# Optimization experiments

Measured on AMD Instinct MI355X. Metric: run time of the kernel, lower is better.

## Reference

```python
import jax, jax.numpy as jnp
import numpy as np

B, N, K = 2, 16384, 8
NH, HD, CH, KV_IN = 4, 32, 128, 128
EPS = 1e-5

def layer_norm(x, g, b):
    mu = x.mean(-1, keepdims=True)
    var = ((x - mu) ** 2).mean(-1, keepdims=True)
    return (x - mu) / jnp.sqrt(var + EPS) * g + b

def setup_inputs() -> dict:
    key = jax.random.key(0)
    ks = jax.random.split(key, 8)
    s = 0.02
    return {
        "query_in": jax.random.normal(ks[0], (B, N, CH), jnp.float32),
        "kv_in": jax.random.normal(ks[1], (B, N, K, KV_IN), jnp.float32),
        "w_kv": jax.random.normal(ks[2], (KV_IN, 2 * NH * HD), jnp.float32) * s,
        "w_q": jax.random.normal(ks[3], (CH, NH * HD), jnp.float32) * s,
        "w_mh": jax.random.normal(ks[4], (NH * HD, CH), jnp.float32) * s,
        "b_mh": jnp.zeros((CH,), jnp.float32),
        "w1": jax.random.normal(ks[5], (CH, CH), jnp.float32) * s,
        "b1": jnp.zeros((CH,), jnp.float32),
        "w2": jax.random.normal(ks[6], (CH, CH), jnp.float32) * s,
        "b2": jnp.zeros((CH,), jnp.float32),
        "ln1_g": jnp.ones((CH,), jnp.float32),
        "ln1_b": jnp.zeros((CH,), jnp.float32),
        "ln2_g": jnp.ones((CH,), jnp.float32),
        "ln2_b": jnp.zeros((CH,), jnp.float32),
    }

def reference(query_in, kv_in, w_kv, w_q, w_mh, b_mh, w1, b1, w2, b2,
              ln1_g, ln1_b, ln2_g, ln2_b):
    # q projection: [B,N,CH] -> [B,N,NH,HD]
    q = (query_in @ w_q).reshape(B, N, NH, HD)
    # kv projection: [B,N,K,KV_IN] -> [B,N,K,2,NH,HD]; chunk(2) on last dim
    kv = (kv_in @ w_kv).reshape(B, N, K, 2, NH, HD)
    k, v = kv[..., 0, :, :], kv[..., 1, :, :]  # each [B,N,K,NH,HD]
    # per-token local attention over its own K keys
    sim = jnp.einsum('bnhd,bnkhd->bnhk', q, k) / np.sqrt(HD).astype(np.float32)
    attn = jax.nn.softmax(sim, axis=-1)
    out = jnp.einsum('bnhk,bnkhd->bnhd', attn, v).reshape(B, N, NH * HD)
    out = out @ w_mh + b_mh
    res = layer_norm(out, ln1_g, ln1_b) + query_in
    # GELU MLP (torch nn.GELU default = exact erf form)
    mlp = jax.nn.gelu(res @ w1 + b1, approximate=False) @ w2 + b2
    return layer_norm(mlp + res, ln2_g, ln2_b)
```

## Files before the change

kernel.cpp:

```cpp
#include <hip/hip_runtime.h>
#include <hip/hip_fp16.h>

typedef _Float16 f16x8 __attribute__((ext_vector_type(8)));
typedef float f32x4 __attribute__((ext_vector_type(4)));
typedef unsigned int uint32;

#define LDW 136
#define TB  32

#define WAITLGKM() do { __builtin_amdgcn_s_waitcnt(0xC07F); __builtin_amdgcn_sched_barrier(0); } while(0)

#define BAR() do {                                          \
  asm volatile("s_waitcnt lgkmcnt(0)" ::: "memory");        \
  __builtin_amdgcn_sched_barrier(0);                        \
  __builtin_amdgcn_s_barrier();                             \
  __builtin_amdgcn_sched_barrier(0);                        \
} while (0)

union F16x8U { f16x8 v; __half2 h2[4]; uint2 u2[2]; uint4 u4; };

__device__ __forceinline__ uint32 pk2f(float a, float b) {
  __half2 h = __floats2half2_rn(a, b);
  return *reinterpret_cast<uint32*>(&h);
}
__device__ __forceinline__ float bcast(float v, int sl) {
  return __int_as_float(__builtin_amdgcn_readlane(__float_as_int(v), sl));
}
template <int CTRL, int RMASK = 0xF, int BMASK = 0xF>
__device__ __forceinline__ float dppmov(float v) {
  return __int_as_float(__builtin_amdgcn_update_dpp(
      0, __float_as_int(v), CTRL, RMASK, BMASK, true));
}
template <int PAT>
__device__ __forceinline__ float swzf(float v) {
  return __int_as_float(__builtin_amdgcn_ds_swizzle(__float_as_int(v), PAT));
}
__device__ __forceinline__ float wred_sum(float v) {
  v += dppmov<0x111>(v);
  v += dppmov<0x112>(v);
  v += dppmov<0x114>(v);
  v += dppmov<0x118>(v);
  v += dppmov<0x142, 0xA>(v);
  v += dppmov<0x143, 0xC>(v);
  return __int_as_float(__builtin_amdgcn_readlane(__float_as_int(v), 63));
}
__device__ __forceinline__ f16x8 ldsv8(const __half* p) {
  return *reinterpret_cast<const f16x8*>(p);
}
__device__ __forceinline__ f32x4 mfma16(f16x8 a, f16x8 b, f32x4 c) {
  return __builtin_amdgcn_mfma_f32_16x16x32_f16(a, b, c, 0, 0, 0);
}
__device__ __forceinline__ void stp(__half* base, int fr, int fq, int nt, f32x4 a) {
  uint2 u; u.x = pk2f(a[0], a[1]); u.y = pk2f(a[2], a[3]);
  *reinterpret_cast<uint2*>(&base[fr * LDW + nt * 16 + fq * 4]) = u;
}

#define OFF_WQ   0
#define OFF_WK2  16384
#define OFF_WV   36864
#define OFF_WMH  53248
#define OFF_W1   69632
#define OFF_W2   86016
#define WS_HALVES 102400

__global__ void prep_weights(const float* __restrict__ wq, const float* __restrict__ wkv,
                             const float* __restrict__ wmh, const float* __restrict__ w1,
                             const float* __restrict__ w2, __half* __restrict__ ws) {
  int idx = blockIdx.x * 256 + threadIdx.x;
  if (idx >= WS_HALVES) return;
  float v;
  if (idx < OFF_WK2) {
    int t = idx, c = t >> 7, k = t & 127;
    v = wq[k * 128 + c];
  } else if (idx < OFF_WV) {
    int t = idx - OFF_WK2;
    int d = t % 40, row = t / 40;
    int h = row >> 7, i = row & 127;
    v = (d < 32) ? wkv[i * 256 + h * 32 + d] : 0.f;
  } else if (idx < OFF_WMH) {
    int t = idx - OFF_WV, c = t >> 7, k = t & 127;
    v = wkv[k * 256 + 128 + c];
  } else if (idx < OFF_W1) {
    int t = idx - OFF_WMH, c = t >> 7, k = t & 127;
    v = wmh[k * 128 + c];
  } else if (idx < OFF_W2) {
    int t = idx - OFF_W1, c = t >> 7, k = t & 127;
    v = w1[k * 128 + c];
  } else {
    int t = idx - OFF_W2, c = t >> 7, k = t & 127;
    v = w2[k * 128 + c];
  }
  ws[idx] = __float2half_rn(v);
}

#define LOADB2(GOFF, NT0, NT1, BF) do {                                          \
  _Pragma("unroll")                                                              \
  for (int t_ = 0; t_ < 2; ++t_) {                                               \
    int nt_ = t_ ? (NT1) : (NT0);                                                \
    _Pragma("unroll")                                                            \
    for (int ks_ = 0; ks_ < 4; ++ks_)                                            \
      BF[t_][ks_] = *reinterpret_cast<const f16x8*>(                             \
          wsv + (GOFF) + (nt_*16 + fr)*128 + ks_*32 + fq*8);                     \
  } } while (0)

#define GEMM2(AT, BF, ACC0, ACC1) do {                                           \
  _Pragma("unroll")                                                              \
  for (int ks_ = 0; ks_ < 4; ++ks_) {                                            \
    f16x8 b_ = ldsv8(&(AT)[fr * LDW + ks_ * 32 + fq * 8]);                       \
    ACC0 = mfma16(BF[0][ks_], b_, ACC0);                                         \
    ACC1 = mfma16(BF[1][ks_], b_, ACC1);                                         \
  } } while (0)

__global__ void __launch_bounds__(256, 3) ca_mfma(
    const float* __restrict__ xq, const float* __restrict__ kvin,
    const __half* __restrict__ wsv,
    const float* __restrict__ bmh, const float* __restrict__ b1,
    const float* __restrict__ b2,
    const float* __restrict__ g1, const float* __restrict__ bb1,
    const float* __restrict__ g2, const float* __restrict__ bb2,
    float* __restrict__ outp)
{
  __shared__ __half QWC[2 * 64 * LDW];
  __shared__ __half UBUF[2 * 32 * LDW];

  const int tid = threadIdx.x;
  const int wv = tid >> 6, lane = tid & 63;
  const int fr = lane & 15, fq = lane >> 4;
  const int tb = blockIdx.x * TB;
  const int ltb = wv * 4;

  __half* const QWs[2] = {QWC, QWC + 64 * LDW};
  __half* const Us[2]  = {UBUF, UBUF + 32 * LDW};

  const f32x4 ZZ = {0.f, 0.f, 0.f, 0.f};

  float4 pre[2][4];
#pragma unroll
  for (int st = 0; st < 2; ++st) {
    const float4* kv4 = reinterpret_cast<const float4*>(
        kvin + (size_t)(tb + st * 16 + ltb) * 1024);
    pre[st][0] = kv4[2 * lane];       pre[st][1] = kv4[2 * lane + 1];
    pre[st][2] = kv4[2 * lane + 128]; pre[st][3] = kv4[2 * lane + 129];
  }
  f16x8 bf[2][4];
  LOADB2(OFF_WQ, wv, 4 + wv, bf);

  {
    int tok = tid >> 4, ko = (tid & 15) * 8;
#pragma unroll
    for (int st = 0; st < 2; ++st) {
      const float4* s0 = reinterpret_cast<const float4*>(
          xq + (size_t)(tb + st * 16 + tok) * 128 + ko);
      float4 a = s0[0], b = s0[1];
      uint4 u; u.x = pk2f(a.x, a.y); u.y = pk2f(a.z, a.w);
      u.z = pk2f(b.x, b.y); u.w = pk2f(b.z, b.w);
      *reinterpret_cast<uint4*>(&Us[st][tok * LDW + ko]) = u;
    }
  }
  BAR();

#pragma unroll
  for (int st = 0; st < 2; ++st) {
    f32x4 aA = ZZ, aB = ZZ;
    GEMM2(Us[st], bf, aA, aB);
    stp(Us[st] + 16 * LDW, fr, fq, wv, aA);
    stp(Us[st] + 16 * LDW, fr, fq, 4 + wv, aB);
  }
  f16x8 bq[8];
#pragma unroll
  for (int nt = 0; nt < 8; ++nt)
    bq[nt] = *reinterpret_cast<const f16x8*>(
        wsv + OFF_WK2 + (wv * 128 + nt * 16 + fr) * 40 + fq * 8);
  BAR();

#pragma unroll
  for (int st = 0; st < 2; ++st) {
    f16x8 aq = ldsv8(&Us[st][16 * LDW + fr * LDW + wv * 32 + fq * 8]);
#pragma unroll
    for (int nt = 0; nt < 8; ++nt) {
      f32x4 acc = mfma16(bq[nt], aq, ZZ);
      uint2 u; u.x = pk2f(acc[0], acc[1]); u.y = pk2f(acc[2], acc[3]);
      *reinterpret_cast<uint2*>(&QWs[st][(wv * 16 + fr) * LDW + nt * 16 + fq * 4]) = u;
    }
  }
  BAR();

  {
    const int kr = lane >> 4, i8 = (lane & 15) * 8;
    const int l2 = 2 * lane;
    const float SCALE = 0.17677669529663687f;
#pragma unroll 1
    for (int lt = 0; lt < 4; ++lt) {
      const int ltok = ltb + lt;
      WAITLGKM();
#pragma unroll
      for (int st = 0; st < 2; ++st) {
        __half* kvw = Us[st] + wv * 1088;
        uint4 u0, u1;
        u0.x = pk2f(pre[st][0].x, pre[st][0].y); u0.y = pk2f(pre[st][0].z, pre[st][0].w);
        u0.z = pk2f(pre[st][1].x, pre[st][1].y); u0.w = pk2f(pre[st][1].z, pre[st][1].w);
        u1.x = pk2f(pre[st][2].x, pre[st][2].y); u1.y = pk2f(pre[st][2].z, pre[st][2].w);
        u1.z = pk2f(pre[st][3].x, pre[st][3].y); u1.w = pk2f(pre[st][3].z, pre[st][3].w);
        *reinterpret_cast<uint4*>(&kvw[kr * LDW + i8]) = u0;
        *reinterpret_cast<uint4*>(&kvw[(4 + kr) * LDW + i8]) = u1;
      }
      if (lt < 3) {
#pragma unroll
        for (int st = 0; st < 2; ++st) {
          const float4* kv4 = reinterpret_cast<const float4*>(
              kvin + (size_t)(tb + st * 16 + ltok + 1) * 1024);
          pre[st][0] = kv4[2 * lane];       pre[st][1] = kv4[2 * lane + 1];
          pre[st][2] = kv4[2 * lane + 128]; pre[st][3] = kv4[2 * lane + 129];
        }
      }
      WAITLGKM();
      f32x4 acc[2];
#pragma unroll
      for (int st = 0; st < 2; ++st) {
        __half* kvw = Us[st] + wv * 1088;
        f32x4 a = ZZ;
#pragma unroll
        for (int ks = 0; ks < 4; ++ks) {
          f16x8 a_ = ldsv8(&QWs[st][((fr & 3) * 16 + ltok) * LDW + ks * 32 + fq * 8]);
          f16x8 b_ = ldsv8(&kvw[(fr & 7) * LDW + ks * 32 + fq * 8]);
          a = mfma16(a_, b_, a);
        }
        acc[st] = a;
      }
      float at_[2][4];
#pragma unroll
      for (int st = 0; st < 2; ++st) {
#pragma unroll
        for (int r = 0; r < 4; ++r) {
          float s = acc[st][r] * SCALE;
          float mx = fmaxf(s, dppmov<0xB1>(s));
          mx = fmaxf(mx, dppmov<0x4E>(mx));
          mx = fmaxf(mx, swzf<0x101F>(mx));
          float e = __expf(s - mx);
          float dn = e + dppmov<0xB1>(e);
          dn += dppmov<0x4E>(dn);
          dn += swzf<0x101F>(dn);
          at_[st][r] = __fdividef(e, dn);
        }
      }
#pragma unroll
      for (int st = 0; st < 2; ++st) {
        __half* kvw = Us[st] + wv * 1088;
        __half2 kvc[8];
#pragma unroll
        for (int k = 0; k < 8; ++k)
          kvc[k] = *reinterpret_cast<const __half2*>(&kvw[k * LDW + l2]);
#pragma unroll
        for (int h = 0; h < 4; ++h) {
          float c0 = 0.f, c1 = 0.f;
#pragma unroll
          for (int k = 0; k < 8; ++k) {
            float a = bcast(at_[st][h], k);
            float2 kf = __half22float2(kvc[k]);
            c0 = fmaf(a, kf.x, c0);
            c1 = fmaf(a, kf.y, c1);
          }
          *reinterpret_cast<__half2*>(&QWs[st][(h * 16 + ltok) * LDW + l2]) =
              __floats2half2_rn(c0, c1);
        }
      }
    }
  }
  LOADB2(OFF_WV, wv, 4 + wv, bf);
  BAR();

  float2 xr[2][4];
#pragma unroll
  for (int st = 0; st < 2; ++st)
#pragma unroll
    for (int lt = 0; lt < 4; ++lt) {
      int tok = tb + st * 16 + ltb + lt;
      xr[st][lt] = *reinterpret_cast<const float2*>(&xq[(size_t)tok * 128 + 2 * lane]);
    }
  {
    const int h1 = wv >> 1, h2 = 2 + (wv >> 1);
#pragma unroll
    for (int st = 0; st < 2; ++st) {
      f32x4 a1c = ZZ, a2c = ZZ;
#pragma unroll
      for (int ks = 0; ks < 4; ++ks) {
        f16x8 b1f = ldsv8(&QWs[st][(h1 * 16 + fr) * LDW + ks * 32 + fq * 8]);
        a1c = mfma16(bf[0][ks], b1f, a1c);
        f16x8 b2f = ldsv8(&QWs[st][(h2 * 16 + fr) * LDW + ks * 32 + fq * 8]);
        a2c = mfma16(bf[1][ks], b2f, a2c);
      }
      stp(Us[st], fr, fq, wv, a1c);
      stp(Us[st], fr, fq, 4 + wv, a2c);
    }
  }
  LOADB2(OFF_WMH, wv, 4 + wv, bf);
  BAR();

#pragma unroll
  for (int st = 0; st < 2; ++st) {
    f32x4 aA = ZZ, aB = ZZ;
    GEMM2(Us[st], bf, aA, aB);
    stp(QWs[st], fr, fq, wv, aA);
    stp(QWs[st], fr, fq, 4 + wv, aB);
  }
  LOADB2(OFF_W1, wv, 4 + wv, bf);
  BAR();

  {
    const int l2 = 2 * lane;
    float2 bm = *reinterpret_cast<const float2*>(&bmh[l2]);
    float2 gg = *reinterpret_cast<const float2*>(&g1[l2]);
    float2 cc = *reinterpret_cast<const float2*>(&bb1[l2]);
#pragma unroll
    for (int st = 0; st < 2; ++st)
#pragma unroll
      for (int lt = 0; lt < 4; ++lt) {
        int row = ltb + lt;
        float2 y = __half22float2(
            *reinterpret_cast<const __half2*>(&QWs[st][row * LDW + l2]));
        float v0 = y.x + bm.x, v1 = y.y + bm.y;
        float s = wred_sum(v0 + v1);
        float sq = wred_sum(v0 * v0 + v1 * v1);
        float mu = s * 0.0078125f;
        float var = sq * 0.0078125f - mu * mu;
        float rstd = rsqrtf(var + 1e-5f);
        float r0 = (v0 - mu) * rstd * gg.x + cc.x + xr[st][lt].x;
        float r1 = (v1 - mu) * rstd * gg.y + cc.y + xr[st][lt].y;
        *reinterpret_cast<__half2*>(&QWs[st][(16 + row) * LDW + l2]) =
            __floats2half2_rn(r0, r1);
      }
  }
  BAR();

  {
    int c0 = wv * 16 + fq * 4, c1 = 64 + wv * 16 + fq * 4;
    float4 b1a = *reinterpret_cast<const float4*>(&b1[c0]);
    float4 b1b = *reinterpret_cast<const float4*>(&b1[c1]);
#pragma unroll
    for (int st = 0; st < 2; ++st) {
      f32x4 aA = ZZ, aB = ZZ;
      GEMM2(QWs[st] + 16 * LDW, bf, aA, aB);
      uint2 ua, ub;
      float t0, t1;
      t0 = aA[0] + b1a.x; t0 = 0.5f * t0 * (1.f + erff(t0 * 0.70710678118654752f));
      t1 = aA[1] + b1a.y; t1 = 0.5f * t1 * (1.f + erff(t1 * 0.70710678118654752f));
      ua.x = pk2f(t0, t1);
      t0 = aA[2] + b1a.z; t0 = 0.5f * t0 * (1.f + erff(t0 * 0.70710678118654752f));
      t1 = aA[3] + b1a.w; t1 = 0.5f * t1 * (1.f + erff(t1 * 0.70710678118654752f));
      ua.y = pk2f(t0, t1);
      t0 = aB[0] + b1b.x; t0 = 0.5f * t0 * (1.f + erff(t0 * 0.70710678118654752f));
      t1 = aB[1] + b1b.y; t1 = 0.5f * t1 * (1.f + erff(t1 * 0.70710678118654752f));
      ub.x = pk2f(t0, t1);
      t0 = aB[2] + b1b.z; t0 = 0.5f * t0 * (1.f + erff(t0 * 0.70710678118654752f));
      t1 = aB[3] + b1b.w; t1 = 0.5f * t1 * (1.f + erff(t1 * 0.70710678118654752f));
      ub.y = pk2f(t0, t1);
      *reinterpret_cast<uint2*>(&QWs[st][(32 + fr) * LDW + c0]) = ua;
      *reinterpret_cast<uint2*>(&QWs[st][(32 + fr) * LDW + c1]) = ub;
    }
  }
  LOADB2(OFF_W2, wv, 4 + wv, bf);
  BAR();

  {
    int c0 = wv * 16 + fq * 4, c1 = 64 + wv * 16 + fq * 4;
    float4 b2a = *reinterpret_cast<const float4*>(&b2[c0]);
    float4 b2b = *reinterpret_cast<const float4*>(&b2[c1]);
#pragma unroll
    for (int st = 0; st < 2; ++st) {
      f32x4 aA = ZZ, aB = ZZ;
      GEMM2(QWs[st] + 32 * LDW, bf, aA, aB);
      F16x8U ra, rb;
      ra.u2[0] = *reinterpret_cast<const uint2*>(&QWs[st][(16 + fr) * LDW + c0]);
      rb.u2[0] = *reinterpret_cast<const uint2*>(&QWs[st][(16 + fr) * LDW + c1]);
      uint2 ua, ub;
      float2 p0 = __half22float2(ra.h2[0]), p1 = __half22float2(ra.h2[1]);
      ua.x = pk2f(aA[0] + b2a.x + p0.x, aA[1] + b2a.y + p0.y);
      ua.y = pk2f(aA[2] + b2a.z + p1.x, aA[3] + b2a.w + p1.y);
      float2 p2 = __half22float2(rb.h2[0]), p3 = __half22float2(rb.h2[1]);
      ub.x = pk2f(aB[0] + b2b.x + p2.x, aB[1] + b2b.y + p2.y);
      ub.y = pk2f(aB[2] + b2b.z + p3.x, aB[3] + b2b.w + p3.y);
      *reinterpret_cast<uint2*>(&QWs[st][(48 + fr) * LDW + c0]) = ua;
      *reinterpret_cast<uint2*>(&QWs[st][(48 + fr) * LDW + c1]) = ub;
    }
  }
  BAR();

  {
    const int l2 = 2 * lane;
    float2 gg = *reinterpret_cast<const float2*>(&g2[l2]);
    float2 cc = *reinterpret_cast<const float2*>(&bb2[l2]);
#pragma unroll
    for (int st = 0; st < 2; ++st)
#pragma unroll
      for (int lt = 0; lt < 4; ++lt) {
        int row = ltb + lt, tok = tb + st * 16 + row;
        float2 v = __half22float2(
            *reinterpret_cast<const __half2*>(&QWs[st][(48 + row) * LDW + l2]));
        float s = wred_sum(v.x + v.y);
        float sq = wred_sum(v.x * v.x + v.y * v.y);
        float mu = s * 0.0078125f;
        float var = sq * 0.0078125f - mu * mu;
        float rstd = rsqrtf(var + 1e-5f);
        float2 o;
        o.x = (v.x - mu) * rstd * gg.x + cc.x;
        o.y = (v.y - mu) * rstd * gg.y + cc.y;
        *reinterpret_cast<float2*>(&outp[(size_t)tok * 128 + l2]) = o;
      }
  }
}

extern "C" void kernel_launch(void* const* d_in, const int* in_sizes, int n_in,
                              void* d_out, int out_size, void* d_ws, size_t ws_size,
                              hipStream_t stream) {
  const float* xq = (const float*)d_in[0];
  const float* kv = (const float*)d_in[1];
  const float* wkv = (const float*)d_in[2];
  const float* wq = (const float*)d_in[3];
  const float* wmh = (const float*)d_in[4];
  const float* bmh = (const float*)d_in[5];
  const float* w1 = (const float*)d_in[6];
  const float* b1 = (const float*)d_in[7];
  const float* w2 = (const float*)d_in[8];
  const float* b2 = (const float*)d_in[9];
  const float* g1 = (const float*)d_in[10];
  const float* bb1 = (const float*)d_in[11];
  const float* g2 = (const float*)d_in[12];
  const float* bb2 = (const float*)d_in[13];
  __half* ws = (__half*)d_ws;

  prep_weights<<<(WS_HALVES + 255) / 256, 256, 0, stream>>>(wq, wkv, wmh, w1, w2, ws);

  const int tokens = 32768;
  ca_mfma<<<tokens / TB, 256, 0, stream>>>(xq, kv, ws, bmh, b1, b2,
                                           g1, bb1, g2, bb2, (float*)d_out);
}
```

Measured before the change: 54.43 us.

## Fuse LayerNorms into MFMA epilogues with cross-wave partial sums in LDS

Both LayerNorms are now computed directly from the MFMA accumulator registers. Each wave reduces its column slice with a swizzle and a shuffle, writes per-row partial sums to a small LDS array, and finalizes after a barrier. This removes the fp16 round-trip through LDS, the separate per-token full-wave DPP reductions and one barrier per LayerNorm. The Q-projection column assignment is changed so each wave produces the columns it consumes next, which lets one block barrier become a local lgkm wait. It also relies on the column mapping being exactly right and adds a small LDS buffer.

```diff
diff --git a/kernel.cpp b/kernel.cpp
--- a/kernel.cpp
+++ b/kernel.cpp
@@ -34,15 +34,6 @@
 template <int PAT>
 __device__ __forceinline__ float swzf(float v) {
   return __int_as_float(__builtin_amdgcn_ds_swizzle(__float_as_int(v), PAT));
-}
-__device__ __forceinline__ float wred_sum(float v) {
-  v += dppmov<0x111>(v);
-  v += dppmov<0x112>(v);
-  v += dppmov<0x114>(v);
-  v += dppmov<0x118>(v);
-  v += dppmov<0x142, 0xA>(v);
-  v += dppmov<0x143, 0xC>(v);
-  return __int_as_float(__builtin_amdgcn_readlane(__float_as_int(v), 63));
 }
 __device__ __forceinline__ f16x8 ldsv8(const __half* p) {
   return *reinterpret_cast<const f16x8*>(p);
@@ -122,12 +113,14 @@
 {
   __shared__ __half QWC[2 * 64 * LDW];
   __shared__ __half UBUF[2 * 32 * LDW];
+  __shared__ float  PART[2][2][16][4];
 
   const int tid = threadIdx.x;
   const int wv = tid >> 6, lane = tid & 63;
   const int fr = lane & 15, fq = lane >> 4;
   const int tb = blockIdx.x * TB;
   const int ltb = wv * 4;
+  const int cA = wv * 16 + fq * 4, cB = 64 + cA;
 
   __half* const QWs[2] = {QWC, QWC + 64 * LDW};
   __half* const Us[2]  = {UBUF, UBUF + 32 * LDW};
@@ -143,7 +136,7 @@
     pre[st][2] = kv4[2 * lane + 128]; pre[st][3] = kv4[2 * lane + 129];
   }
   f16x8 bf[2][4];
-  LOADB2(OFF_WQ, wv, 4 + wv, bf);
+  LOADB2(OFF_WQ, 2 * wv, 2 * wv + 1, bf);
 
   {
     int tok = tid >> 4, ko = (tid & 15) * 8;
@@ -163,15 +156,15 @@
   for (int st = 0; st < 2; ++st) {
     f32x4 aA = ZZ, aB = ZZ;
     GEMM2(Us[st], bf, aA, aB);
-    stp(Us[st] + 16 * LDW, fr, fq, wv, aA);
-    stp(Us[st] + 16 * LDW, fr, fq, 4 + wv, aB);
+    stp(Us[st] + 16 * LDW, fr, fq, 2 * wv, aA);
+    stp(Us[st] + 16 * LDW, fr, fq, 2 * wv + 1, aB);
   }
   f16x8 bq[8];
 #pragma unroll
   for (int nt = 0; nt < 8; ++nt)
     bq[nt] = *reinterpret_cast<const f16x8*>(
         wsv + OFF_WK2 + (wv * 128 + nt * 16 + fr) * 40 + fq * 8);
-  BAR();
+  WAITLGKM();
 
 #pragma unroll
   for (int st = 0; st < 2; ++st) {
@@ -269,14 +262,6 @@
   LOADB2(OFF_WV, wv, 4 + wv, bf);
   BAR();
 
-  float2 xr[2][4];
-#pragma unroll
-  for (int st = 0; st < 2; ++st)
-#pragma unroll
-    for (int lt = 0; lt < 4; ++lt) {
-      int tok = tb + st * 16 + ltb + lt;
-      xr[st][lt] = *reinterpret_cast<const float2*>(&xq[(size_t)tok * 128 + 2 * lane]);
-    }
   {
     const int h1 = wv >> 1, h2 = 2 + (wv >> 1);
 #pragma unroll
@@ -294,48 +279,72 @@
     }
   }
   LOADB2(OFF_WMH, wv, 4 + wv, bf);
-  BAR();
-
+  float4 xqA[2], xqB[2];
 #pragma unroll
   for (int st = 0; st < 2; ++st) {
-    f32x4 aA = ZZ, aB = ZZ;
-    GEMM2(Us[st], bf, aA, aB);
-    stp(QWs[st], fr, fq, wv, aA);
-    stp(QWs[st], fr, fq, 4 + wv, aB);
+    const float* xrow = xq + (size_t)(tb + st * 16 + fr) * 128;
+    xqA[st] = *reinterpret_cast<const float4*>(xrow + cA);
+    xqB[st] = *reinterpret_cast<const float4*>(xrow + cB);
+  }
+  BAR();
+
+  float vv[2][8];
+  {
+    float4 bmA = *reinterpret_cast<const float4*>(&bmh[cA]);
+    float4 bmB = *reinterpret_cast<const float4*>(&bmh[cB]);
+#pragma unroll
+    for (int st = 0; st < 2; ++st) {
+      f32x4 aA = ZZ, aB = ZZ;
+      GEMM2(Us[st], bf, aA, aB);
+      vv[st][0] = aA[0] + bmA.x; vv[st][1] = aA[1] + bmA.y;
+      vv[st][2] = aA[2] + bmA.z; vv[st][3] = aA[3] + bmA.w;
+      vv[st][4] = aB[0] + bmB.x; vv[st][5] = aB[1] + bmB.y;
+      vv[st][6] = aB[2] + bmB.z; vv[st][7] = aB[3] + bmB.w;
+      float s = 0.f, sq = 0.f;
+#pragma unroll
+      for (int r = 0; r < 8; ++r) { s += vv[st][r]; sq = fmaf(vv[st][r], vv[st][r], sq); }
+      s += swzf<0x401F>(s);  s += __shfl_xor(s, 32);
+      sq += swzf<0x401F>(sq); sq += __shfl_xor(sq, 32);
+      if (fq == 0) { PART[st][0][fr][wv] = s; PART[st][1][fr][wv] = sq; }
+    }
   }
   LOADB2(OFF_W1, wv, 4 + wv, bf);
   BAR();
 
   {
-    const int l2 = 2 * lane;
-    float2 bm = *reinterpret_cast<const float2*>(&bmh[l2]);
-    float2 gg = *reinterpret_cast<const float2*>(&g1[l2]);
-    float2 cc = *reinterpret_cast<const float2*>(&bb1[l2]);
-#pragma unroll
-    for (int st = 0; st < 2; ++st)
-#pragma unroll
-      for (int lt = 0; lt < 4; ++lt) {
-        int row = ltb + lt;
-        float2 y = __half22float2(
-            *reinterpret_cast<const __half2*>(&QWs[st][row * LDW + l2]));
-        float v0 = y.x + bm.x, v1 = y.y + bm.y;
-        float s = wred_sum(v0 + v1);
-        float sq = wred_sum(v0 * v0 + v1 * v1);
-        float mu = s * 0.0078125f;
-        float var = sq * 0.0078125f - mu * mu;
-        float rstd = rsqrtf(var + 1e-5f);
-        float r0 = (v0 - mu) * rstd * gg.x + cc.x + xr[st][lt].x;
-        float r1 = (v1 - mu) * rstd * gg.y + cc.y + xr[st][lt].y;
-        *reinterpret_cast<__half2*>(&QWs[st][(16 + row) * LDW + l2]) =
-            __floats2half2_rn(r0, r1);
-      }
-  }
-  BAR();
-
-  {
-    int c0 = wv * 16 + fq * 4, c1 = 64 + wv * 16 + fq * 4;
-    float4 b1a = *reinterpret_cast<const float4*>(&b1[c0]);
-    float4 b1b = *reinterpret_cast<const float4*>(&b1[c1]);
+    float4 gA = *reinterpret_cast<const float4*>(&g1[cA]);
+    float4 gB = *reinterpret_cast<const float4*>(&g1[cB]);
+    float4 cAv = *reinterpret_cast<const float4*>(&bb1[cA]);
+    float4 cBv = *reinterpret_cast<const float4*>(&bb1[cB]);
+#pragma unroll
+    for (int st = 0; st < 2; ++st) {
+      float4 ps = *reinterpret_cast<const float4*>(&PART[st][0][fr][0]);
+      float4 pq = *reinterpret_cast<const float4*>(&PART[st][1][fr][0]);
+      float su = (ps.x + ps.y) + (ps.z + ps.w);
+      float squ = (pq.x + pq.y) + (pq.z + pq.w);
+      float mu = su * 0.0078125f;
+      float var = squ * 0.0078125f - mu * mu;
+      float rstd = rsqrtf(var + 1e-5f);
+      float rA0 = (vv[st][0] - mu) * rstd * gA.x + cAv.x + xqA[st].x;
+      float rA1 = (vv[st][1] - mu) * rstd * gA.y + cAv.y + xqA[st].y;
+      float rA2 = (vv[st][2] - mu) * rstd * gA.z + cAv.z + xqA[st].z;
+      float rA3 = (vv[st][3] - mu) * rstd * gA.w + cAv.w + xqA[st].w;
+      float rB0 = (vv[st][4] - mu) * rstd * gB.x + cBv.x + xqB[st].x;
+      float rB1 = (vv[st][5] - mu) * rstd * gB.y + cBv.y + xqB[st].y;
+      float rB2 = (vv[st][6] - mu) * rstd * gB.z + cBv.z + xqB[st].z;
+      float rB3 = (vv[st][7] - mu) * rstd * gB.w + cBv.w + xqB[st].w;
+      uint2 ua, ub;
+      ua.x = pk2f(rA0, rA1); ua.y = pk2f(rA2, rA3);
+      ub.x = pk2f(rB0, rB1); ub.y = pk2f(rB2, rB3);
+      *reinterpret_cast<uint2*>(&QWs[st][(16 + fr) * LDW + cA]) = ua;
+      *reinterpret_cast<uint2*>(&QWs[st][(16 + fr) * LDW + cB]) = ub;
+    }
+  }
+  BAR();
+
+  {
+    float4 b1a = *reinterpret_cast<const float4*>(&b1[cA]);
+    float4 b1b = *reinterpret_cast<const float4*>(&b1[cB]);
 #pragma unroll
     for (int st = 0; st < 2; ++st) {
       f32x4 aA = ZZ, aB = ZZ;
@@ -354,58 +363,67 @@
       t0 = aB[2] + b1b.z; t0 = 0.5f * t0 * (1.f + erff(t0 * 0.70710678118654752f));
       t1 = aB[3] + b1b.w; t1 = 0.5f * t1 * (1.f + erff(t1 * 0.70710678118654752f));
       ub.y = pk2f(t0, t1);
-      *reinterpret_cast<uint2*>(&QWs[st][(32 + fr) * LDW + c0]) = ua;
-      *reinterpret_cast<uint2*>(&QWs[st][(32 + fr) * LDW + c1]) = ub;
+      *reinterpret_cast<uint2*>(&QWs[st][(32 + fr) * LDW + cA]) = ua;
+      *reinterpret_cast<uint2*>(&QWs[st][(32 + fr) * LDW + cB]) = ub;
     }
   }
   LOADB2(OFF_W2, wv, 4 + wv, bf);
   BAR();
 
-  {
-    int c0 = wv * 16 + fq * 4, c1 = 64 + wv * 16 + fq * 4;
-    float4 b2a = *reinterpret_cast<const float4*>(&b2[c0]);
-    float4 b2b = *reinterpret_cast<const float4*>(&b2[c1]);
+  float ww[2][8];
+  {
+    float4 b2a = *reinterpret_cast<const float4*>(&b2[cA]);
+    float4 b2b = *reinterpret_cast<const float4*>(&b2[cB]);
 #pragma unroll
     for (int st = 0; st < 2; ++st) {
       f32x4 aA = ZZ, aB = ZZ;
       GEMM2(QWs[st] + 32 * LDW, bf, aA, aB);
       F16x8U ra, rb;
-      ra.u2[0] = *reinterpret_cast<const uint2*>(&QWs[st][(16 + fr) * LDW + c0]);
-      rb.u2[0] = *reinterpret_cast<const uint2*>(&QWs[st][(16 + fr) * LDW + c1]);
-      uint2 ua, ub;
+      ra.u2[0] = *reinterpret_cast<const uint2*>(&QWs[st][(16 + fr) * LDW + cA]);
+      rb.u2[0] = *reinterpret_cast<const uint2*>(&QWs[st][(16 + fr) * LDW + cB]);
       float2 p0 = __half22float2(ra.h2[0]), p1 = __half22float2(ra.h2[1]);
-      ua.x = pk2f(aA[0] + b2a.x + p0.x, aA[1] + b2a.y + p0.y);
-      ua.y = pk2f(aA[2] + b2a.z + p1.x, aA[3] + b2a.w + p1.y);
       float2 p2 = __half22float2(rb.h2[0]), p3 = __half22float2(rb.h2[1]);
-      ub.x = pk2f(aB[0] + b2b.x + p2.x, aB[1] + b2b.y + p2.y);
-      ub.y = pk2f(aB[2] + b2b.z + p3.x, aB[3] + b2b.w + p3.y);
-      *reinterpret_cast<uint2*>(&QWs[st][(48 + fr) * LDW + c0]) = ua;
-      *reinterpret_cast<uint2*>(&QWs[st][(48 + fr) * LDW + c1]) = ub;
-    }
-  }
-  BAR();
-
-  {
-    const int l2 = 2 * lane;
-    float2 gg = *reinterpret_cast<const float2*>(&g2[l2]);
-    float2 cc = *reinterpret_cast<const float2*>(&bb2[l2]);
-#pragma unroll
-    for (int st = 0; st < 2; ++st)
-#pragma unroll
-      for (int lt = 0; lt < 4; ++lt) {
-        int row = ltb + lt, tok = tb + st * 16 + row;
-        float2 v = __half22float2(
-            *reinterpret_cast<const __half2*>(&QWs[st][(48 + row) * LDW + l2]));
-        float s = wred_sum(v.x + v.y);
-        float sq = wred_sum(v.x * v.x + v.y * v.y);
-        float mu = s * 0.0078125f;
-        float var = sq * 0.0078125f - mu * mu;
-        float rstd = rsqrtf(var + 1e-5f);
-        float2 o;
-        o.x = (v.x - mu) * rstd * gg.x + cc.x;
-        o.y = (v.y - mu) * rstd * gg.y + cc.y;
-        *reinterpret_cast<float2*>(&outp[(size_t)tok * 128 + l2]) = o;
-      }
+      ww[st][0] = aA[0] + b2a.x + p0.x; ww[st][1] = aA[1] + b2a.y + p0.y;
+      ww[st][2] = aA[2] + b2a.z + p1.x; ww[st][3] = aA[3] + b2a.w + p1.y;
+      ww[st][4] = aB[0] + b2b.x + p2.x; ww[st][5] = aB[1] + b2b.y + p2.y;
+      ww[st][6] = aB[2] + b2b.z + p3.x; ww[st][7] = aB[3] + b2b.w + p3.y;
+      float s = 0.f, sq = 0.f;
+#pragma unroll
+      for (int r = 0; r < 8; ++r) { s += ww[st][r]; sq = fmaf(ww[st][r], ww[st][r], sq); }
+      s += swzf<0x401F>(s);  s += __shfl_xor(s, 32);
+      sq += swzf<0x401F>(sq); sq += __shfl_xor(sq, 32);
+      if (fq == 0) { PART[st][0][fr][wv] = s; PART[st][1][fr][wv] = sq; }
+    }
+  }
+  BAR();
+
+  {
+    float4 gA = *reinterpret_cast<const float4*>(&g2[cA]);
+    float4 gB = *reinterpret_cast<const float4*>(&g2[cB]);
+    float4 cAv = *reinterpret_cast<const float4*>(&bb2[cA]);
+    float4 cBv = *reinterpret_cast<const float4*>(&bb2[cB]);
+#pragma unroll
+    for (int st = 0; st < 2; ++st) {
+      float4 ps = *reinterpret_cast<const float4*>(&PART[st][0][fr][0]);
+      float4 pq = *reinterpret_cast<const float4*>(&PART[st][1][fr][0]);
+      float su = (ps.x + ps.y) + (ps.z + ps.w);
+      float squ = (pq.x + pq.y) + (pq.z + pq.w);
+      float mu = su * 0.0078125f;
+      float var = squ * 0.0078125f - mu * mu;
+      float rstd = rsqrtf(var + 1e-5f);
+      float4 oA, oB;
+      oA.x = (ww[st][0] - mu) * rstd * gA.x + cAv.x;
+      oA.y = (ww[st][1] - mu) * rstd * gA.y + cAv.y;
+      oA.z = (ww[st][2] - mu) * rstd * gA.z + cAv.z;
+      oA.w = (ww[st][3] - mu) * rstd * gA.w + cAv.w;
+      oB.x = (ww[st][4] - mu) * rstd * gB.x + cBv.x;
+      oB.y = (ww[st][5] - mu) * rstd * gB.y + cBv.y;
+      oB.z = (ww[st][6] - mu) * rstd * gB.z + cBv.z;
+      oB.w = (ww[st][7] - mu) * rstd * gB.w + cBv.w;
+      float* orow = outp + (size_t)(tb + st * 16 + fr) * 128;
+      *reinterpret_cast<float4*>(orow + cA) = oA;
+      *reinterpret_cast<float4*>(orow + cB) = oB;
+    }
   }
 }
 
```

Result: no change. 53.77 us (-1.2%).

## Restructure fused kernel into single-wave blocks of eight tokens without barriers

Applied to the files above, without the earlier changes.

Replaces the 256-thread, 32-token block with a 64-thread, single-wave block that handles 8 tokens, so the block barriers go away and LDS use per block shrinks. Each wave now does every GEMM itself, reading full weight tiles from global memory/L2 instead of splitting output columns across waves. LayerNorm is done from MFMA accumulators in registers using swizzle and shuffle reductions. In exchange, half of each 16-row MFMA tile is wasted (only 8 tokens are live), and weight traffic per token from L2 rises sharply.

```diff
diff --git a/kernel.cpp b/kernel.cpp
--- a/kernel.cpp
+++ b/kernel.cpp
@@ -6,16 +6,8 @@
 typedef unsigned int uint32;
 
 #define LDW 136
-#define TB  32
 
 #define WAITLGKM() do { __builtin_amdgcn_s_waitcnt(0xC07F); __builtin_amdgcn_sched_barrier(0); } while(0)
-
-#define BAR() do {                                          \
-  asm volatile("s_waitcnt lgkmcnt(0)" ::: "memory");        \
-  __builtin_amdgcn_sched_barrier(0);                        \
-  __builtin_amdgcn_s_barrier();                             \
-  __builtin_amdgcn_sched_barrier(0);                        \
-} while (0)
 
 union F16x8U { f16x8 v; __half2 h2[4]; uint2 u2[2]; uint4 u4; };
 
@@ -35,22 +27,13 @@
 __device__ __forceinline__ float swzf(float v) {
   return __int_as_float(__builtin_amdgcn_ds_swizzle(__float_as_int(v), PAT));
 }
-__device__ __forceinline__ float wred_sum(float v) {
-  v += dppmov<0x111>(v);
-  v += dppmov<0x112>(v);
-  v += dppmov<0x114>(v);
-  v += dppmov<0x118>(v);
-  v += dppmov<0x142, 0xA>(v);
-  v += dppmov<0x143, 0xC>(v);
-  return __int_as_float(__builtin_amdgcn_readlane(__float_as_int(v), 63));
-}
 __device__ __forceinline__ f16x8 ldsv8(const __half* p) {
   return *reinterpret_cast<const f16x8*>(p);
 }
 __device__ __forceinline__ f32x4 mfma16(f16x8 a, f16x8 b, f32x4 c) {
   return __builtin_amdgcn_mfma_f32_16x16x32_f16(a, b, c, 0, 0, 0);
 }
-__device__ __forceinline__ void stp(__half* base, int fr, int fq, int nt, f32x4 a) {
+__device__ __forceinline__ void stp8(__half* base, int fr, int fq, int nt, f32x4 a) {
   uint2 u; u.x = pk2f(a[0], a[1]); u.y = pk2f(a[2], a[3]);
   *reinterpret_cast<uint2*>(&base[fr * LDW + nt * 16 + fq * 4]) = u;
 }
@@ -93,25 +76,7 @@
   ws[idx] = __float2half_rn(v);
 }
 
-#define LOADB2(GOFF, NT0, NT1, BF) do {                                          \
-  _Pragma("unroll")                                                              \
-  for (int t_ = 0; t_ < 2; ++t_) {                                               \
-    int nt_ = t_ ? (NT1) : (NT0);                                                \
-    _Pragma("unroll")                                                            \
-    for (int ks_ = 0; ks_ < 4; ++ks_)                                            \
-      BF[t_][ks_] = *reinterpret_cast<const f16x8*>(                             \
-          wsv + (GOFF) + (nt_*16 + fr)*128 + ks_*32 + fq*8);                     \
-  } } while (0)
-
-#define GEMM2(AT, BF, ACC0, ACC1) do {                                           \
-  _Pragma("unroll")                                                              \
-  for (int ks_ = 0; ks_ < 4; ++ks_) {                                            \
-    f16x8 b_ = ldsv8(&(AT)[fr * LDW + ks_ * 32 + fq * 8]);                       \
-    ACC0 = mfma16(BF[0][ks_], b_, ACC0);                                         \
-    ACC1 = mfma16(BF[1][ks_], b_, ACC1);                                         \
-  } } while (0)
-
-__global__ void __launch_bounds__(256, 3) ca_mfma(
+__global__ void __launch_bounds__(64, 3) ca_wave(
     const float* __restrict__ xq, const float* __restrict__ kvin,
     const __half* __restrict__ wsv,
     const float* __restrict__ bmh, const float* __restrict__ b1,
@@ -120,119 +85,118 @@
     const float* __restrict__ g2, const float* __restrict__ bb2,
     float* __restrict__ outp)
 {
-  __shared__ __half QWC[2 * 64 * LDW];
-  __shared__ __half UBUF[2 * 32 * LDW];
-
-  const int tid = threadIdx.x;
-  const int wv = tid >> 6, lane = tid & 63;
+  __shared__ __half WS[48 * LDW];
+
+  const int lane = threadIdx.x;
   const int fr = lane & 15, fq = lane >> 4;
-  const int tb = blockIdx.x * TB;
-  const int ltb = wv * 4;
-
-  __half* const QWs[2] = {QWC, QWC + 64 * LDW};
-  __half* const Us[2]  = {UBUF, UBUF + 32 * LDW};
+  const int fr8 = fr & 7;
+  const bool act = fr < 8;
+  const int wtok = blockIdx.x * 8;
+
+  __half* qwp = WS;
+  __half* arA = WS + 32 * LDW;
+  __half* arB = WS + 40 * LDW;
 
   const f32x4 ZZ = {0.f, 0.f, 0.f, 0.f};
+  const float SCALE = 0.17677669529663687f;
 
   float4 pre[2][4];
 #pragma unroll
   for (int st = 0; st < 2; ++st) {
-    const float4* kv4 = reinterpret_cast<const float4*>(
-        kvin + (size_t)(tb + st * 16 + ltb) * 1024);
+    const float4* kv4 = reinterpret_cast<const float4*>(kvin + (size_t)(wtok + st) * 1024);
     pre[st][0] = kv4[2 * lane];       pre[st][1] = kv4[2 * lane + 1];
     pre[st][2] = kv4[2 * lane + 128]; pre[st][3] = kv4[2 * lane + 129];
   }
-  f16x8 bf[2][4];
-  LOADB2(OFF_WQ, wv, 4 + wv, bf);
-
-  {
-    int tok = tid >> 4, ko = (tid & 15) * 8;
-#pragma unroll
-    for (int st = 0; st < 2; ++st) {
-      const float4* s0 = reinterpret_cast<const float4*>(
-          xq + (size_t)(tb + st * 16 + tok) * 128 + ko);
-      float4 a = s0[0], b = s0[1];
-      uint4 u; u.x = pk2f(a.x, a.y); u.y = pk2f(a.z, a.w);
-      u.z = pk2f(b.x, b.y); u.w = pk2f(b.z, b.w);
-      *reinterpret_cast<uint4*>(&Us[st][tok * LDW + ko]) = u;
-    }
-  }
-  BAR();
-
-#pragma unroll
-  for (int st = 0; st < 2; ++st) {
-    f32x4 aA = ZZ, aB = ZZ;
-    GEMM2(Us[st], bf, aA, aB);
-    stp(Us[st] + 16 * LDW, fr, fq, wv, aA);
-    stp(Us[st] + 16 * LDW, fr, fq, 4 + wv, aB);
-  }
-  f16x8 bq[8];
-#pragma unroll
-  for (int nt = 0; nt < 8; ++nt)
-    bq[nt] = *reinterpret_cast<const f16x8*>(
-        wsv + OFF_WK2 + (wv * 128 + nt * 16 + fr) * 40 + fq * 8);
-  BAR();
-
-#pragma unroll
-  for (int st = 0; st < 2; ++st) {
-    f16x8 aq = ldsv8(&Us[st][16 * LDW + fr * LDW + wv * 32 + fq * 8]);
-#pragma unroll
-    for (int nt = 0; nt < 8; ++nt) {
-      f32x4 acc = mfma16(bq[nt], aq, ZZ);
-      uint2 u; u.x = pk2f(acc[0], acc[1]); u.y = pk2f(acc[2], acc[3]);
-      *reinterpret_cast<uint2*>(&QWs[st][(wv * 16 + fr) * LDW + nt * 16 + fq * 4]) = u;
-    }
-  }
-  BAR();
-
-  {
-    const int kr = lane >> 4, i8 = (lane & 15) * 8;
-    const int l2 = 2 * lane;
-    const float SCALE = 0.17677669529663687f;
+
+#pragma unroll
+  for (int c = 0; c < 2; ++c) {
+    int idx = lane + c * 64;
+    int tok = idx >> 4, ko = (idx & 15) * 8;
+    const float4* s0 = reinterpret_cast<const float4*>(xq + (size_t)(wtok + tok) * 128 + ko);
+    float4 a = s0[0], b = s0[1];
+    uint4 u; u.x = pk2f(a.x, a.y); u.y = pk2f(a.z, a.w);
+    u.z = pk2f(b.x, b.y); u.w = pk2f(b.z, b.w);
+    *reinterpret_cast<uint4*>(&arA[tok * LDW + ko]) = u;
+  }
+  WAITLGKM();
+
+  {
+    f16x8 bx[4];
+#pragma unroll
+    for (int ks = 0; ks < 4; ++ks) bx[ks] = ldsv8(&arA[fr8 * LDW + ks * 32 + fq * 8]);
+#pragma unroll
+    for (int nt = 0; nt < 8; ++nt) {
+      f32x4 acc = ZZ;
+#pragma unroll
+      for (int ks = 0; ks < 4; ++ks) {
+        f16x8 a_ = *reinterpret_cast<const f16x8*>(
+            wsv + OFF_WQ + (nt * 16 + fr) * 128 + ks * 32 + fq * 8);
+        acc = mfma16(a_, bx[ks], acc);
+      }
+      if (act) stp8(arB, fr, fq, nt, acc);
+    }
+  }
+  WAITLGKM();
+
+#pragma unroll
+  for (int h = 0; h < 4; ++h) {
+    f16x8 aq = ldsv8(&arB[fr8 * LDW + h * 32 + fq * 8]);
+#pragma unroll
+    for (int nt = 0; nt < 8; ++nt) {
+      f16x8 a_ = *reinterpret_cast<const f16x8*>(
+          wsv + OFF_WK2 + (size_t)((h * 128 + nt * 16 + fr) * 40 + fq * 8));
+      f32x4 acc = mfma16(a_, aq, ZZ);
+      if (act) {
+        uint2 u; u.x = pk2f(acc[0], acc[1]); u.y = pk2f(acc[2], acc[3]);
+        *reinterpret_cast<uint2*>(&qwp[(h * 8 + fr) * LDW + nt * 16 + fq * 4]) = u;
+      }
+    }
+  }
+
+  {
+    const int kr = lane >> 4, i8v = (lane & 15) * 8, l2 = 2 * lane;
+    __half* const kvs[2] = {arA, arB};
 #pragma unroll 1
-    for (int lt = 0; lt < 4; ++lt) {
-      const int ltok = ltb + lt;
+    for (int t2 = 0; t2 < 4; ++t2) {
       WAITLGKM();
 #pragma unroll
       for (int st = 0; st < 2; ++st) {
-        __half* kvw = Us[st] + wv * 1088;
         uint4 u0, u1;
         u0.x = pk2f(pre[st][0].x, pre[st][0].y); u0.y = pk2f(pre[st][0].z, pre[st][0].w);
         u0.z = pk2f(pre[st][1].x, pre[st][1].y); u0.w = pk2f(pre[st][1].z, pre[st][1].w);
         u1.x = pk2f(pre[st][2].x, pre[st][2].y); u1.y = pk2f(pre[st][2].z, pre[st][2].w);
         u1.z = pk2f(pre[st][3].x, pre[st][3].y); u1.w = pk2f(pre[st][3].z, pre[st][3].w);
-        *reinterpret_cast<uint4*>(&kvw[kr * LDW + i8]) = u0;
-        *reinterpret_cast<uint4*>(&kvw[(4 + kr) * LDW + i8]) = u1;
-      }
-      if (lt < 3) {
+        *reinterpret_cast<uint4*>(&kvs[st][kr * LDW + i8v]) = u0;
+        *reinterpret_cast<uint4*>(&kvs[st][(4 + kr) * LDW + i8v]) = u1;
+      }
+      if (t2 < 3) {
 #pragma unroll
         for (int st = 0; st < 2; ++st) {
           const float4* kv4 = reinterpret_cast<const float4*>(
-              kvin + (size_t)(tb + st * 16 + ltok + 1) * 1024);
+              kvin + (size_t)(wtok + 2 * t2 + 2 + st) * 1024);
           pre[st][0] = kv4[2 * lane];       pre[st][1] = kv4[2 * lane + 1];
           pre[st][2] = kv4[2 * lane + 128]; pre[st][3] = kv4[2 * lane + 129];
         }
       }
       WAITLGKM();
-      f32x4 acc[2];
+      f32x4 sim[2];
 #pragma unroll
       for (int st = 0; st < 2; ++st) {
-        __half* kvw = Us[st] + wv * 1088;
         f32x4 a = ZZ;
 #pragma unroll
         for (int ks = 0; ks < 4; ++ks) {
-          f16x8 a_ = ldsv8(&QWs[st][((fr & 3) * 16 + ltok) * LDW + ks * 32 + fq * 8]);
-          f16x8 b_ = ldsv8(&kvw[(fr & 7) * LDW + ks * 32 + fq * 8]);
+          f16x8 a_ = ldsv8(&qwp[((fr & 3) * 8 + 2 * t2 + st) * LDW + ks * 32 + fq * 8]);
+          f16x8 b_ = ldsv8(&kvs[st][fr8 * LDW + ks * 32 + fq * 8]);
           a = mfma16(a_, b_, a);
         }
-        acc[st] = a;
+        sim[st] = a;
       }
       float at_[2][4];
 #pragma unroll
       for (int st = 0; st < 2; ++st) {
 #pragma unroll
         for (int r = 0; r < 4; ++r) {
-          float s = acc[st][r] * SCALE;
+          float s = sim[st][r] * SCALE;
           float mx = fmaxf(s, dppmov<0xB1>(s));
           mx = fmaxf(mx, dppmov<0x4E>(mx));
           mx = fmaxf(mx, swzf<0x101F>(mx));
@@ -245,11 +209,10 @@
       }
 #pragma unroll
       for (int st = 0; st < 2; ++st) {
-        __half* kvw = Us[st] + wv * 1088;
         __half2 kvc[8];
 #pragma unroll
         for (int k = 0; k < 8; ++k)
-          kvc[k] = *reinterpret_cast<const __half2*>(&kvw[k * LDW + l2]);
+          kvc[k] = *reinterpret_cast<const __half2*>(&kvs[st][k * LDW + l2]);
 #pragma unroll
         for (int h = 0; h < 4; ++h) {
           float c0 = 0.f, c1 = 0.f;
@@ -260,152 +223,154 @@
             c0 = fmaf(a, kf.x, c0);
             c1 = fmaf(a, kf.y, c1);
           }
-          *reinterpret_cast<__half2*>(&QWs[st][(h * 16 + ltok) * LDW + l2]) =
+          *reinterpret_cast<__half2*>(&qwp[(h * 8 + 2 * t2 + st) * LDW + l2]) =
               __floats2half2_rn(c0, c1);
         }
       }
     }
   }
-  LOADB2(OFF_WV, wv, 4 + wv, bf);
-  BAR();
-
-  float2 xr[2][4];
-#pragma unroll
-  for (int st = 0; st < 2; ++st)
-#pragma unroll
-    for (int lt = 0; lt < 4; ++lt) {
-      int tok = tb + st * 16 + ltb + lt;
-      xr[st][lt] = *reinterpret_cast<const float2*>(&xq[(size_t)tok * 128 + 2 * lane]);
-    }
-  {
-    const int h1 = wv >> 1, h2 = 2 + (wv >> 1);
-#pragma unroll
-    for (int st = 0; st < 2; ++st) {
-      f32x4 a1c = ZZ, a2c = ZZ;
+  WAITLGKM();
+
+#pragma unroll
+  for (int h = 0; h < 4; ++h) {
+    f16x8 bc[4];
+#pragma unroll
+    for (int ks = 0; ks < 4; ++ks)
+      bc[ks] = ldsv8(&qwp[(h * 8 + fr8) * LDW + ks * 32 + fq * 8]);
+#pragma unroll
+    for (int j = 0; j < 2; ++j) {
+      int nt = 2 * h + j;
+      f32x4 acc = ZZ;
 #pragma unroll
       for (int ks = 0; ks < 4; ++ks) {
-        f16x8 b1f = ldsv8(&QWs[st][(h1 * 16 + fr) * LDW + ks * 32 + fq * 8]);
-        a1c = mfma16(bf[0][ks], b1f, a1c);
-        f16x8 b2f = ldsv8(&QWs[st][(h2 * 16 + fr) * LDW + ks * 32 + fq * 8]);
-        a2c = mfma16(bf[1][ks], b2f, a2c);
-      }
-      stp(Us[st], fr, fq, wv, a1c);
-      stp(Us[st], fr, fq, 4 + wv, a2c);
-    }
-  }
-  LOADB2(OFF_WMH, wv, 4 + wv, bf);
-  BAR();
-
-#pragma unroll
-  for (int st = 0; st < 2; ++st) {
-    f32x4 aA = ZZ, aB = ZZ;
-    GEMM2(Us[st], bf, aA, aB);
-    stp(QWs[st], fr, fq, wv, aA);
-    stp(QWs[st], fr, fq, 4 + wv, aB);
-  }
-  LOADB2(OFF_W1, wv, 4 + wv, bf);
-  BAR();
-
-  {
-    const int l2 = 2 * lane;
-    float2 bm = *reinterpret_cast<const float2*>(&bmh[l2]);
-    float2 gg = *reinterpret_cast<const float2*>(&g1[l2]);
-    float2 cc = *reinterpret_cast<const float2*>(&bb1[l2]);
-#pragma unroll
-    for (int st = 0; st < 2; ++st)
-#pragma unroll
-      for (int lt = 0; lt < 4; ++lt) {
-        int row = ltb + lt;
-        float2 y = __half22float2(
-            *reinterpret_cast<const __half2*>(&QWs[st][row * LDW + l2]));
-        float v0 = y.x + bm.x, v1 = y.y + bm.y;
-        float s = wred_sum(v0 + v1);
-        float sq = wred_sum(v0 * v0 + v1 * v1);
-        float mu = s * 0.0078125f;
-        float var = sq * 0.0078125f - mu * mu;
-        float rstd = rsqrtf(var + 1e-5f);
-        float r0 = (v0 - mu) * rstd * gg.x + cc.x + xr[st][lt].x;
-        float r1 = (v1 - mu) * rstd * gg.y + cc.y + xr[st][lt].y;
-        *reinterpret_cast<__half2*>(&QWs[st][(16 + row) * LDW + l2]) =
-            __floats2half2_rn(r0, r1);
-      }
-  }
-  BAR();
-
-  {
-    int c0 = wv * 16 + fq * 4, c1 = 64 + wv * 16 + fq * 4;
-    float4 b1a = *reinterpret_cast<const float4*>(&b1[c0]);
-    float4 b1b = *reinterpret_cast<const float4*>(&b1[c1]);
-#pragma unroll
-    for (int st = 0; st < 2; ++st) {
-      f32x4 aA = ZZ, aB = ZZ;
-      GEMM2(QWs[st] + 16 * LDW, bf, aA, aB);
-      uint2 ua, ub;
+        f16x8 a_ = *reinterpret_cast<const f16x8*>(
+            wsv + OFF_WV + (nt * 16 + fr) * 128 + ks * 32 + fq * 8);
+        acc = mfma16(a_, bc[ks], acc);
+      }
+      if (act) stp8(arA, fr, fq, nt, acc);
+    }
+  }
+  float4 xr[8];
+#pragma unroll
+  for (int nt = 0; nt < 8; ++nt)
+    xr[nt] = *reinterpret_cast<const float4*>(
+        xq + (size_t)(wtok + fr8) * 128 + nt * 16 + fq * 4);
+  WAITLGKM();
+
+  float vv[32];
+  {
+    f16x8 bo[4];
+#pragma unroll
+    for (int ks = 0; ks < 4; ++ks) bo[ks] = ldsv8(&arA[fr8 * LDW + ks * 32 + fq * 8]);
+#pragma unroll
+    for (int nt = 0; nt < 8; ++nt) {
+      f32x4 acc = ZZ;
+#pragma unroll
+      for (int ks = 0; ks < 4; ++ks) {
+        f16x8 a_ = *reinterpret_cast<const f16x8*>(
+            wsv + OFF_WMH + (nt * 16 + fr) * 128 + ks * 32 + fq * 8);
+        acc = mfma16(a_, bo[ks], acc);
+      }
+      float4 bm = *reinterpret_cast<const float4*>(&bmh[nt * 16 + fq * 4]);
+      vv[nt * 4 + 0] = acc[0] + bm.x; vv[nt * 4 + 1] = acc[1] + bm.y;
+      vv[nt * 4 + 2] = acc[2] + bm.z; vv[nt * 4 + 3] = acc[3] + bm.w;
+    }
+  }
+  {
+    float s = 0.f, sq = 0.f;
+#pragma unroll
+    for (int r = 0; r < 32; ++r) { s += vv[r]; sq = fmaf(vv[r], vv[r], sq); }
+    s += swzf<0x401F>(s);  s += __shfl_xor(s, 32);
+    sq += swzf<0x401F>(sq); sq += __shfl_xor(sq, 32);
+    float mu = s * 0.0078125f;
+    float var = sq * 0.0078125f - mu * mu;
+    float rstd = rsqrtf(var + 1e-5f);
+#pragma unroll
+    for (int nt = 0; nt < 8; ++nt) {
+      float4 g = *reinterpret_cast<const float4*>(&g1[nt * 16 + fq * 4]);
+      float4 c = *reinterpret_cast<const float4*>(&bb1[nt * 16 + fq * 4]);
+      float r0 = (vv[nt * 4 + 0] - mu) * rstd * g.x + c.x + xr[nt].x;
+      float r1 = (vv[nt * 4 + 1] - mu) * rstd * g.y + c.y + xr[nt].y;
+      float r2 = (vv[nt * 4 + 2] - mu) * rstd * g.z + c.z + xr[nt].z;
+      float r3 = (vv[nt * 4 + 3] - mu) * rstd * g.w + c.w + xr[nt].w;
+      uint2 u; u.x = pk2f(r0, r1); u.y = pk2f(r2, r3);
+      if (act) *reinterpret_cast<uint2*>(&arB[fr * LDW + nt * 16 + fq * 4]) = u;
+    }
+  }
+  WAITLGKM();
+
+  {
+    f16x8 br[4];
+#pragma unroll
+    for (int ks = 0; ks < 4; ++ks) br[ks] = ldsv8(&arB[fr8 * LDW + ks * 32 + fq * 8]);
+#pragma unroll
+    for (int nt = 0; nt < 8; ++nt) {
+      f32x4 acc = ZZ;
+#pragma unroll
+      for (int ks = 0; ks < 4; ++ks) {
+        f16x8 a_ = *reinterpret_cast<const f16x8*>(
+            wsv + OFF_W1 + (nt * 16 + fr) * 128 + ks * 32 + fq * 8);
+        acc = mfma16(a_, br[ks], acc);
+      }
+      float4 bb = *reinterpret_cast<const float4*>(&b1[nt * 16 + fq * 4]);
       float t0, t1;
-      t0 = aA[0] + b1a.x; t0 = 0.5f * t0 * (1.f + erff(t0 * 0.70710678118654752f));
-      t1 = aA[1] + b1a.y; t1 = 0.5f * t1 * (1.f + erff(t1 * 0.70710678118654752f));
-      ua.x = pk2f(t0, t1);
-      t0 = aA[2] + b1a.z; t0 = 0.5f * t0 * (1.f + erff(t0 * 0.70710678118654752f));
-      t1 = aA[3] + b1a.w; t1 = 0.5f * t1 * (1.f + erff(t1 * 0.70710678118654752f));
-      ua.y = pk2f(t0, t1);
-      t0 = aB[0] + b1b.x; t0 = 0.5f * t0 * (1.f + erff(t0 * 0.70710678118654752f));
-      t1 = aB[1] + b1b.y; t1 = 0.5f * t1 * (1.f + erff(t1 * 0.70710678118654752f));
-      ub.x = pk2f(t0, t1);
-      t0 = aB[2] + b1b.z; t0 = 0.5f * t0 * (1.f + erff(t0 * 0.70710678118654752f));
-      t1 = aB[3] + b1b.w; t1 = 0.5f * t1 * (1.f + erff(t1 * 0.70710678118654752f));
-      ub.y = pk2f(t0, t1);
-      *reinterpret_cast<uint2*>(&QWs[st][(32 + fr) * LDW + c0]) = ua;
-      *reinterpret_cast<uint2*>(&QWs[st][(32 + fr) * LDW + c1]) = ub;
-    }
-  }
-  LOADB2(OFF_W2, wv, 4 + wv, bf);
-  BAR();
-
-  {
-    int c0 = wv * 16 + fq * 4, c1 = 64 + wv * 16 + fq * 4;
-    float4 b2a = *reinterpret_cast<const float4*>(&b2[c0]);
-    float4 b2b = *reinterpret_cast<const float4*>(&b2[c1]);
-#pragma unroll
-    for (int st = 0; st < 2; ++st) {
-      f32x4 aA = ZZ, aB = ZZ;
-      GEMM2(QWs[st] + 32 * LDW, bf, aA, aB);
-      F16x8U ra, rb;
-      ra.u2[0] = *reinterpret_cast<const uint2*>(&QWs[st][(16 + fr) * LDW + c0]);
-      rb.u2[0] = *reinterpret_cast<const uint2*>(&QWs[st][(16 + fr) * LDW + c1]);
-      uint2 ua, ub;
-      float2 p0 = __half22float2(ra.h2[0]), p1 = __half22float2(ra.h2[1]);
-      ua.x = pk2f(aA[0] + b2a.x + p0.x, aA[1] + b2a.y + p0.y);
-      ua.y = pk2f(aA[2] + b2a.z + p1.x, aA[3] + b2a.w + p1.y);
-      float2 p2 = __half22float2(rb.h2[0]), p3 = __half22float2(rb.h2[1]);
-      ub.x = pk2f(aB[0] + b2b.x + p2.x, aB[1] + b2b.y + p2.y);
-      ub.y = pk2f(aB[2] + b2b.z + p3.x, aB[3] + b2b.w + p3.y);
-      *reinterpret_cast<uint2*>(&QWs[st][(48 + fr) * LDW + c0]) = ua;
-      *reinterpret_cast<uint2*>(&QWs[st][(48 + fr) * LDW + c1]) = ub;
-    }
-  }
-  BAR();
-
-  {
-    const int l2 = 2 * lane;
-    float2 gg = *reinterpret_cast<const float2*>(&g2[l2]);
-    float2 cc = *reinterpret_cast<const float2*>(&bb2[l2]);
-#pragma unroll
-    for (int st = 0; st < 2; ++st)
-#pragma unroll
-      for (int lt = 0; lt < 4; ++lt) {
-        int row = ltb + lt, tok = tb + st * 16 + row;
-        float2 v = __half22float2(
-            *reinterpret_cast<const __half2*>(&QWs[st][(48 + row) * LDW + l2]));
-        float s = wred_sum(v.x + v.y);
-        float sq = wred_sum(v.x * v.x + v.y * v.y);
-        float mu = s * 0.0078125f;
-        float var = sq * 0.0078125f - mu * mu;
-        float rstd = rsqrtf(var + 1e-5f);
-        float2 o;
-        o.x = (v.x - mu) * rstd * gg.x + cc.x;
-        o.y = (v.y - mu) * rstd * gg.y + cc.y;
-        *reinterpret_cast<float2*>(&outp[(size_t)tok * 128 + l2]) = o;
-      }
+      uint2 u;
+      t0 = acc[0] + bb.x; t0 = 0.5f * t0 * (1.f + erff(t0 * 0.70710678118654752f));
+      t1 = acc[1] + bb.y; t1 = 0.5f * t1 * (1.f + erff(t1 * 0.70710678118654752f));
+      u.x = pk2f(t0, t1);
+      t0 = acc[2] + bb.z; t0 = 0.5f * t0 * (1.f + erff(t0 * 0.70710678118654752f));
+      t1 = acc[3] + bb.w; t1 = 0.5f * t1 * (1.f + erff(t1 * 0.70710678118654752f));
+      u.y = pk2f(t0, t1);
+      if (act) *reinterpret_cast<uint2*>(&arA[fr * LDW + nt * 16 + fq * 4]) = u;
+    }
+  }
+  WAITLGKM();
+
+  float ww[32];
+  {
+    f16x8 bh[4];
+#pragma unroll
+    for (int ks = 0; ks < 4; ++ks) bh[ks] = ldsv8(&arA[fr8 * LDW + ks * 32 + fq * 8]);
+#pragma unroll
+    for (int nt = 0; nt < 8; ++nt) {
+      f32x4 acc = ZZ;
+#pragma unroll
+      for (int ks = 0; ks < 4; ++ks) {
+        f16x8 a_ = *reinterpret_cast<const f16x8*>(
+            wsv + OFF_W2 + (nt * 16 + fr) * 128 + ks * 32 + fq * 8);
+        acc = mfma16(a_, bh[ks], acc);
+      }
+      float4 bb = *reinterpret_cast<const float4*>(&b2[nt * 16 + fq * 4]);
+      F16x8U rr;
+      rr.u2[0] = *reinterpret_cast<const uint2*>(&arB[fr8 * LDW + nt * 16 + fq * 4]);
+      float2 p0 = __half22float2(rr.h2[0]), p1 = __half22float2(rr.h2[1]);
+      ww[nt * 4 + 0] = acc[0] + bb.x + p0.x;
+      ww[nt * 4 + 1] = acc[1] + bb.y + p0.y;
+      ww[nt * 4 + 2] = acc[2] + bb.z + p1.x;
+      ww[nt * 4 + 3] = acc[3] + bb.w + p1.y;
+    }
+  }
+  {
+    float s = 0.f, sq = 0.f;
+#pragma unroll
+    for (int r = 0; r < 32; ++r) { s += ww[r]; sq = fmaf(ww[r], ww[r], sq); }
+    s += swzf<0x401F>(s);  s += __shfl_xor(s, 32);
+    sq += swzf<0x401F>(sq); sq += __shfl_xor(sq, 32);
+    float mu = s * 0.0078125f;
+    float var = sq * 0.0078125f - mu * mu;
+    float rstd = rsqrtf(var + 1e-5f);
+    float* orow = outp + (size_t)(wtok + fr8) * 128;
+#pragma unroll
+    for (int nt = 0; nt < 8; ++nt) {
+      float4 g = *reinterpret_cast<const float4*>(&g2[nt * 16 + fq * 4]);
+      float4 c = *reinterpret_cast<const float4*>(&bb2[nt * 16 + fq * 4]);
+      float4 o;
+      o.x = (ww[nt * 4 + 0] - mu) * rstd * g.x + c.x;
+      o.y = (ww[nt * 4 + 1] - mu) * rstd * g.y + c.y;
+      o.z = (ww[nt * 4 + 2] - mu) * rstd * g.z + c.z;
+      o.w = (ww[nt * 4 + 3] - mu) * rstd * g.w + c.w;
+      if (act) *reinterpret_cast<float4*>(orow + nt * 16 + fq * 4) = o;
+    }
   }
 }
 
@@ -418,8 +383,8 @@
   const float* wq = (const float*)d_in[3];
   const float* wmh = (const float*)d_in[4];
   const float* bmh = (const float*)d_in[5];
+  const float* b1 = (const float*)d_in[7];
   const float* w1 = (const float*)d_in[6];
-  const float* b1 = (const float*)d_in[7];
   const float* w2 = (const float*)d_in[8];
   const float* b2 = (const float*)d_in[9];
   const float* g1 = (const float*)d_in[10];
@@ -431,6 +396,6 @@
   prep_weights<<<(WS_HALVES + 255) / 256, 256, 0, stream>>>(wq, wkv, wmh, w1, w2, ws);
 
   const int tokens = 32768;
-  ca_mfma<<<tokens / TB, 256, 0, stream>>>(xq, kv, ws, bmh, b1, b2,
-                                           g1, bb1, g2, bb2, (float*)d_out);
-}
+  ca_wave<<<tokens / 8, 64, 0, stream>>>(xq, kv, ws, bmh, b1, b2,
+                                         g1, bb1, g2, bb2, (float*)d_out);
+}
```

Result: slower. 135.3 us (+148.7%).
